# Kernel tuning notes

Measured on AMD Instinct MI355X. Metric: run time of the kernel, lower is better.

Reference implementation:

```python
import jax, jax.numpy as jnp
import numpy as np

DIM, C_HID, N_HEADS = 128, 32, 4
INF = 1.0e9
LN_EPS = 1e-5


def setup_inputs() -> dict:
    key = jax.random.key(0)
    ks = jax.random.split(key, 10)
    B, I, J, C, H, D = 1, 256, 256, DIM, N_HEADS, C_HID
    s = 0.02
    return {
        "x": jax.random.normal(ks[0], (B, I, J, C), jnp.float32),
        "mask": jnp.ones((B, I, J), jnp.float32),
        "ln_w": jnp.ones((C,), jnp.float32),
        "ln_b": jnp.zeros((C,), jnp.float32),
        "tri_w": jax.random.normal(ks[1], (C, H), jnp.float32) * s,  # bias=False
        "q_w": jax.random.normal(ks[2], (C, H * D), jnp.float32) * s,
        "k_w": jax.random.normal(ks[3], (C, H * D), jnp.float32) * s,
        "v_w": jax.random.normal(ks[4], (C, H * D), jnp.float32) * s,
        "g_w": jax.random.normal(ks[5], (C, H * D), jnp.float32) * s,
        "g_b": jnp.ones((H * D,), jnp.float32),  # gating init: bias=1
        "o_w": jax.random.normal(ks[6], (H * D, C), jnp.float32) * s,
        "o_b": jnp.zeros((C,), jnp.float32),
    }


def _layer_norm(x, w, b):
    mu = jnp.mean(x, axis=-1, keepdims=True)
    var = jnp.mean(jnp.square(x - mu), axis=-1, keepdims=True)
    return (x - mu) * jax.lax.rsqrt(var + LN_EPS) * w + b


def reference(x, mask, ln_w, ln_b, tri_w, q_w, k_w, v_w, g_w, g_b, o_w, o_b):
    # starting=True: no transpose. x: [B, I, J, C], mask: [B, I, J]
    B, I, J, C = x.shape
    H, D = N_HEADS, C_HID
    xn = _layer_norm(x, ln_w, ln_b)

    # mask bias: [B, I, 1, 1, J]; triangle bias: [B, 1, H, I(J), J]
    mask_bias = (INF * (mask - 1.0))[:, :, None, None, :]
    tri_bias = jnp.einsum("bijc,ch->bhij", xn, tri_w)[:, None]

    def proj(w):  # [B, I, H, J, D]
        return (xn @ w).reshape(B, I, J, H, D).transpose(0, 1, 3, 2, 4)

    q = proj(q_w) * (D ** -0.5)
    k = proj(k_w)
    v = proj(v_w)

    logits = jnp.einsum("bihqd,bihkd->bihqk", q, k) + mask_bias + tri_bias
    a = jax.nn.softmax(logits, axis=-1)
    o = jnp.einsum("bihqk,bihkd->bihqd", a, v).transpose(0, 1, 3, 2, 4)  # [B,I,J,H,D]

    g = jax.nn.sigmoid(xn @ g_w + g_b).reshape(B, I, J, H, D)
    o = (o * g).reshape(B, I, J, H * D)
    return o @ o_w + o_b
```

## Files before the change

### kernel.cpp

```cpp
#include <hip/hip_runtime.h>
#include <hip/hip_bf16.h>
#include <math.h>

#define LOG2E_ 1.4426950408889634f

typedef short short8 __attribute__((ext_vector_type(8)));
typedef float f32x4 __attribute__((ext_vector_type(4)));
typedef int int4v __attribute__((ext_vector_type(4)));

#if defined(__has_builtin)
#if __has_builtin(__builtin_amdgcn_exp2f)
#define EXP2F(x) __builtin_amdgcn_exp2f(x)
#else
#define EXP2F(x) exp2f(x)
#endif
#else
#define EXP2F(x) exp2f(x)
#endif

static __device__ __forceinline__ unsigned short f2bf(float f) {
    union { float f; unsigned int u; } c; c.f = f;
    c.u += 0x7fffu + ((c.u >> 16) & 1u);
    return (unsigned short)(c.u >> 16);
}
static __device__ __forceinline__ int pk2bf(float a, float b) {
    union { __hip_bfloat162 h; int i; } u;
    u.h = __float22bfloat162_rn(make_float2(a, b));
    return u.i;
}
static __device__ __forceinline__ void load_lds16(const void* g, void* l) {
    __builtin_amdgcn_global_load_lds(
        (const __attribute__((address_space(1))) void*)g,
        (__attribute__((address_space(3))) void*)l, 16, 0, 0);
}

__global__ __launch_bounds__(256) void ln_prep_kernel(
    const float* __restrict__ x, const float* __restrict__ ln_w,
    const float* __restrict__ ln_b, const float* __restrict__ tri_w,
    const float* __restrict__ qw, const float* __restrict__ kw,
    const float* __restrict__ vw, const float* __restrict__ gw,
    const float* __restrict__ ow,
    unsigned short* __restrict__ xn, float* __restrict__ triT,
    char* __restrict__ wimg)
{
    const int bid = blockIdx.x, tid = threadIdx.x;
    if (bid >= 8192) {
        int id = (bid - 8192) * 256 + tid;
        int h = id / 2688;
        int b = (id - h * 2688) * 16;
        unsigned short v[8];
        if (b < 32768) {
            int sl = b >> 13;
            int bi = b & 8191;
            int row = bi >> 8;
            int c8 = ((bi >> 4) & 15) ^ (row & 7);
            const float* src = (sl == 0) ? qw : (sl == 1) ? kw : (sl == 2) ? vw : gw;
            float scale = (sl == 0) ? (0.17677669529663687f * LOG2E_) : 1.0f;
            int R = h * 32 + row;
            #pragma unroll
            for (int e = 0; e < 8; ++e)
                v[e] = f2bf(src[(c8 * 8 + e) * 128 + R] * scale);
        } else {
            int o = b - 32768;
            int n = o / 80;
            int k8 = (o - n * 80) >> 4;
            if (k8 < 4) {
                #pragma unroll
                for (int e = 0; e < 8; ++e)
                    v[e] = f2bf(ow[(h * 32 + k8 * 8 + e) * 128 + n]);
            } else {
                #pragma unroll
                for (int e = 0; e < 8; ++e) v[e] = 0;
            }
        }
        *(short8*)(wimg + h * 43008 + b) = *(short8*)v;
        return;
    }

    const int row = bid * 8 + (tid >> 5);
    const int l = tid & 31;

    float4 xv = *(const float4*)(x + (size_t)row * 128 + l * 4);
    float s = (xv.x + xv.y) + (xv.z + xv.w);
    #pragma unroll
    for (int mk = 16; mk >= 1; mk >>= 1) s += __shfl_xor(s, mk, 64);
    float mu = s * (1.0f / 128.0f);

    float d0 = xv.x - mu, d1 = xv.y - mu, d2 = xv.z - mu, d3 = xv.w - mu;
    float sq = (d0 * d0 + d1 * d1) + (d2 * d2 + d3 * d3);
    #pragma unroll
    for (int mk = 16; mk >= 1; mk >>= 1) sq += __shfl_xor(sq, mk, 64);
    float rstd = rsqrtf(sq * (1.0f / 128.0f) + 1e-5f);

    float4 wv = *(const float4*)(ln_w + l * 4);
    float4 bv = *(const float4*)(ln_b + l * 4);
    float n0 = d0 * rstd * wv.x + bv.x;
    float n1 = d1 * rstd * wv.y + bv.y;
    float n2 = d2 * rstd * wv.z + bv.z;
    float n3 = d3 * rstd * wv.w + bv.w;

    ushort4 xo;
    xo.x = f2bf(n0); xo.y = f2bf(n1); xo.z = f2bf(n2); xo.w = f2bf(n3);
    *(ushort4*)(xn + (size_t)row * 128 + l * 4) = xo;

    float4 t0 = *(const float4*)(tri_w + (l * 4 + 0) * 4);
    float4 t1 = *(const float4*)(tri_w + (l * 4 + 1) * 4);
    float4 t2 = *(const float4*)(tri_w + (l * 4 + 2) * 4);
    float4 t3 = *(const float4*)(tri_w + (l * 4 + 3) * 4);
    float ax = (n0 * t0.x + n1 * t1.x) + (n2 * t2.x + n3 * t3.x);
    float ay = (n0 * t0.y + n1 * t1.y) + (n2 * t2.y + n3 * t3.y);
    float az = (n0 * t0.z + n1 * t1.z) + (n2 * t2.z + n3 * t3.z);
    float aw = (n0 * t0.w + n1 * t1.w) + (n2 * t2.w + n3 * t3.w);
    #pragma unroll
    for (int mk = 16; mk >= 1; mk >>= 1) {
        ax += __shfl_xor(ax, mk, 64);
        ay += __shfl_xor(ay, mk, 64);
        az += __shfl_xor(az, mk, 64);
        aw += __shfl_xor(aw, mk, 64);
    }
    if (l < 4) {
        float v = (l == 0) ? ax : (l == 1) ? ay : (l == 2) ? az : aw;
        int q = row >> 8, kc = row & 255;
        int off = l * 65536 + (q >> 4) * 4096 + (kc >> 4) * 256
                + (q & 15) * 16 + (kc & 15);
        triT[off] = v * LOG2E_;
    }
}

__global__ __launch_bounds__(1024, 4) void mega_kernel(
    const unsigned short* __restrict__ xn, const char* __restrict__ wimg,
    const float* __restrict__ g_b, const float* __restrict__ mask,
    const float* __restrict__ triT, const float* __restrict__ o_b,
    float* __restrict__ out)
{
    __shared__ __align__(16) char WBUF[2 * 43008];
    __shared__ __align__(16) unsigned short Qg[256 * 36];
    __shared__ __align__(16) unsigned short Kl[256 * 36];
    __shared__ __align__(16) unsigned short Vc[32 * 264];
    __shared__ float mb[256];

    const int i = blockIdx.x;
    const int tid = threadIdx.x;
    const int w = tid >> 6, lane = tid & 63, g = lane >> 4, m = lane & 15;
    const f32x4 zero = {0.f, 0.f, 0.f, 0.f};

    short8 xa[4];
    #pragma unroll
    for (int kc = 0; kc < 4; ++kc)
        xa[kc] = *(const short8*)(xn + (size_t)(i * 256 + w * 16 + m) * 128
                                  + kc * 32 + 8 * g);
    if (tid < 256) mb[tid] = (mask[i * 256 + tid] - 1.0f) * (1.0e9f * LOG2E_);

    {
        const char* src = wimg + w * 1024 + lane * 16;
        char* dst = WBUF + w * 1024;
        load_lds16(src, dst);
        load_lds16(src + 16384, dst + 16384);
        if (w < 10) load_lds16(src + 32768, dst + 32768);
    }
    __syncthreads();

    const int srcA = ((g & 1) << 1) | (g >> 1);
    const int idxA = (srcA * 16 + m) * 4;
    const int idxB = idxA ^ 64;
    const bool low = (lane < 32);
    const bool odd = (g & 1);
    const char* VcB0 = (const char*)Vc + m * 528;
    const char* VcB1 = (const char*)Vc + (16 + m) * 528;

    f32x4 oacc[8];
    #pragma unroll
    for (int nt = 0; nt < 8; ++nt) oacc[nt] = zero;

    const int qrow = w * 16 + m;

    #pragma unroll 1
    for (int h = 0; h < 4; ++h) {
        const char* wb = WBUF + (h & 1) * 43008;

        {
            f32x4 aq[2] = {zero, zero}, ak[2] = {zero, zero};
            #pragma unroll
            for (int kc = 0; kc < 4; ++kc) {
                short8 b0[2], b1[2];
                #pragma unroll
                for (int nt = 0; nt < 2; ++nt) {
                    int row = nt * 16 + m;
                    int off = (row * 256 + kc * 64 + 16 * g) ^ ((row & 7) << 4);
                    b0[nt] = *(const short8*)(wb + off);
                    b1[nt] = *(const short8*)(wb + 8192 + off);
                }
                __builtin_amdgcn_s_setprio(1);
                #pragma unroll
                for (int nt = 0; nt < 2; ++nt) {
                    aq[nt] = __builtin_amdgcn_mfma_f32_16x16x32_bf16(b0[nt], xa[kc], aq[nt], 0, 0, 0);
                    ak[nt] = __builtin_amdgcn_mfma_f32_16x16x32_bf16(b1[nt], xa[kc], ak[nt], 0, 0, 0);
                }
                __builtin_amdgcn_s_setprio(0);
            }
            #pragma unroll
            for (int nt = 0; nt < 2; ++nt) {
                int col = nt * 16 + 4 * g;
                ushort4 q4, k4;
                q4.x = f2bf(aq[nt][0]); q4.y = f2bf(aq[nt][1]);
                q4.z = f2bf(aq[nt][2]); q4.w = f2bf(aq[nt][3]);
                k4.x = f2bf(ak[nt][0]); k4.y = f2bf(ak[nt][1]);
                k4.z = f2bf(ak[nt][2]); k4.w = f2bf(ak[nt][3]);
                *(ushort4*)(Qg + qrow * 36 + col) = q4;
                *(ushort4*)(Kl + qrow * 36 + col) = k4;
            }
        }

        f32x4 gacc[2];
        {
            f32x4 av4[2] = {zero, zero}, ag[2] = {zero, zero};
            #pragma unroll
            for (int kc = 0; kc < 4; ++kc) {
                short8 b0[2], b1[2];
                #pragma unroll
                for (int nt = 0; nt < 2; ++nt) {
                    int row = nt * 16 + m;
                    int off = (row * 256 + kc * 64 + 16 * g) ^ ((row & 7) << 4);
                    b0[nt] = *(const short8*)(wb + 16384 + off);
                    b1[nt] = *(const short8*)(wb + 24576 + off);
                }
                __builtin_amdgcn_s_setprio(1);
                #pragma unroll
                for (int nt = 0; nt < 2; ++nt) {
                    av4[nt] = __builtin_amdgcn_mfma_f32_16x16x32_bf16(xa[kc], b0[nt], av4[nt], 0, 0, 0);
                    ag[nt]  = __builtin_amdgcn_mfma_f32_16x16x32_bf16(b1[nt], xa[kc], ag[nt], 0, 0, 0);
                }
                __builtin_amdgcn_s_setprio(0);
            }
            #pragma unroll
            for (int nt = 0; nt < 2; ++nt) {
                ushort4 v4;
                v4.x = f2bf(av4[nt][0]); v4.y = f2bf(av4[nt][1]);
                v4.z = f2bf(av4[nt][2]); v4.w = f2bf(av4[nt][3]);
                *(ushort4*)(Vc + (nt * 16 + m) * 264 + w * 16 + 4 * g) = v4;
                int col = nt * 16 + 4 * g;
                #pragma unroll
                for (int r = 0; r < 4; ++r)
                    gacc[nt][r] = 1.0f / (1.0f + __expf(-(ag[nt][r] + g_b[h * 32 + col + r])));
            }
        }
        __syncthreads();

        if (h < 3) {
            const char* src = wimg + (h + 1) * 43008 + w * 1024 + lane * 16;
            char* dst = WBUF + ((h + 1) & 1) * 43008 + w * 1024;
            load_lds16(src, dst);
            load_lds16(src + 16384, dst + 16384);
            if (w < 10) load_lds16(src + 32768, dst + 32768);
        }

        const short8 qf = *(const short8*)((const char*)Qg + qrow * 72 + 16 * g);
        const float* triQ = triT + h * 65536 + w * 4096 + m * 16 + 4 * g;

        float ls = 0.f;
        f32x4 o0 = zero, o1 = zero;

        #pragma unroll
        for (int c = 0; c < 8; ++c) {
            int d00, d01, d10, d11;
            {
                const int kt = 2 * c;
                short8 af = *(const short8*)((const char*)Kl + (kt * 16 + m) * 72 + 16 * g);
                f32x4 bias = *(const f32x4*)(mb + kt * 16 + 4 * g)
                           + *(const f32x4*)(triQ + kt * 256);
                __builtin_amdgcn_s_setprio(1);
                f32x4 acc = __builtin_amdgcn_mfma_f32_16x16x32_bf16(af, qf, bias, 0, 0, 0);
                __builtin_amdgcn_s_setprio(0);
                float p0 = EXP2F(acc[0]);
                float p1 = EXP2F(acc[1]);
                float p2 = EXP2F(acc[2]);
                float p3 = EXP2F(acc[3]);
                ls += (p0 + p1) + (p2 + p3);
                d00 = pk2bf(p0, p1); d01 = pk2bf(p2, p3);
            }
            {
                const int kt = 2 * c + 1;
                short8 af = *(const short8*)((const char*)Kl + (kt * 16 + m) * 72 + 16 * g);
                f32x4 bias = *(const f32x4*)(mb + kt * 16 + 4 * g)
                           + *(const f32x4*)(triQ + kt * 256);
                __builtin_amdgcn_s_setprio(1);
                f32x4 acc = __builtin_amdgcn_mfma_f32_16x16x32_bf16(af, qf, bias, 0, 0, 0);
                __builtin_amdgcn_s_setprio(0);
                float p0 = EXP2F(acc[0]);
                float p1 = EXP2F(acc[1]);
                float p2 = EXP2F(acc[2]);
                float p3 = EXP2F(acc[3]);
                ls += (p0 + p1) + (p2 + p3);
                d10 = pk2bf(p0, p1); d11 = pk2bf(p2, p3);
            }
            int pk0 = odd ? d10 : d00;
            int pk1 = odd ? d11 : d01;
            int pk2 = odd ? d00 : d10;
            int pk3 = odd ? d01 : d11;

            int dA0 = __builtin_amdgcn_ds_bpermute(idxA, pk0);
            int dA1 = __builtin_amdgcn_ds_bpermute(idxA, pk1);
            int dB0 = __builtin_amdgcn_ds_bpermute(idxB, pk2);
            int dB1 = __builtin_amdgcn_ds_bpermute(idxB, pk3);
            int4v bi;
            bi.x = low ? dA0 : dB0;
            bi.y = low ? dA1 : dB1;
            bi.z = low ? dB0 : dA0;
            bi.w = low ? dB1 : dA1;
            short8 bs = __builtin_bit_cast(short8, bi);

            short8 av0 = *(const short8*)(VcB0 + c * 64 + 16 * g);
            short8 av1 = *(const short8*)(VcB1 + c * 64 + 16 * g);
            __builtin_amdgcn_s_setprio(1);
            o0 = __builtin_amdgcn_mfma_f32_16x16x32_bf16(av0, bs, o0, 0, 0, 0);
            o1 = __builtin_amdgcn_mfma_f32_16x16x32_bf16(av1, bs, o1, 0, 0, 0);
            __builtin_amdgcn_s_setprio(0);
        }
        ls += __shfl_xor(ls, 16, 64);
        ls += __shfl_xor(ls, 32, 64);
        float inv = 1.0f / ls;

        ushort4 s0, s1;
        s0.x = f2bf(o0[0] * inv * gacc[0][0]);
        s0.y = f2bf(o0[1] * inv * gacc[0][1]);
        s0.z = f2bf(o0[2] * inv * gacc[0][2]);
        s0.w = f2bf(o0[3] * inv * gacc[0][3]);
        s1.x = f2bf(o1[0] * inv * gacc[1][0]);
        s1.y = f2bf(o1[1] * inv * gacc[1][1]);
        s1.z = f2bf(o1[2] * inv * gacc[1][2]);
        s1.w = f2bf(o1[3] * inv * gacc[1][3]);
        *(ushort4*)(Qg + qrow * 36 + 4 * g) = s0;
        *(ushort4*)(Qg + qrow * 36 + 16 + 4 * g) = s1;

        {
            short8 a = *(const short8*)((const char*)Qg + qrow * 72 + 16 * g);
            __builtin_amdgcn_s_setprio(1);
            #pragma unroll
            for (int nt = 0; nt < 8; ++nt) {
                short8 b = *(const short8*)(wb + 32768 + (nt * 16 + m) * 80 + 16 * g);
                oacc[nt] = __builtin_amdgcn_mfma_f32_16x16x32_bf16(b, a, oacc[nt], 0, 0, 0);
            }
            __builtin_amdgcn_s_setprio(0);
        }
        __syncthreads();
    }

    const int orow = i * 256 + qrow;
    #pragma unroll
    for (int nt = 0; nt < 8; ++nt) {
        int col = nt * 16 + 4 * g;
        float4 bv = *(const float4*)(o_b + col);
        float4 o;
        o.x = oacc[nt][0] + bv.x;
        o.y = oacc[nt][1] + bv.y;
        o.z = oacc[nt][2] + bv.z;
        o.w = oacc[nt][3] + bv.w;
        *(float4*)(out + (size_t)orow * 128 + col) = o;
    }
}

extern "C" void kernel_launch(void* const* d_in, const int* in_sizes, int n_in,
                              void* d_out, int out_size, void* d_ws, size_t ws_size,
                              hipStream_t stream) {
    (void)in_sizes; (void)n_in; (void)out_size; (void)ws_size;
    const float* x    = (const float*)d_in[0];
    const float* mask = (const float*)d_in[1];
    const float* ln_w = (const float*)d_in[2];
    const float* ln_b = (const float*)d_in[3];
    const float* tri_w= (const float*)d_in[4];
    const float* q_w  = (const float*)d_in[5];
    const float* k_w  = (const float*)d_in[6];
    const float* v_w  = (const float*)d_in[7];
    const float* g_w  = (const float*)d_in[8];
    const float* g_b  = (const float*)d_in[9];
    const float* o_w  = (const float*)d_in[10];
    const float* o_b  = (const float*)d_in[11];

    char* ws = (char*)d_ws;
    unsigned short* xn  = (unsigned short*)(ws);
    float*          tri = (float*)(ws + 16777216);
    char*           wimg= (char*)(ws + 17825792);

    ln_prep_kernel<<<8234, 256, 0, stream>>>(x, ln_w, ln_b, tri_w,
                                             q_w, k_w, v_w, g_w, o_w,
                                             xn, tri, wimg);
    mega_kernel<<<256, 1024, 0, stream>>>(xn, wimg, g_b, mask, tri, o_b,
                                          (float*)d_out);
}
```

Baseline: 69.74 us.

## Fuse layernorm and weight prep into mega kernel with cooperative grid sync

After: 111.4 us. +59.8%, slower.

```diff
diff --git a/kernel.cpp b/kernel.cpp
--- a/kernel.cpp
+++ b/kernel.cpp
@@ -1,6 +1,9 @@
 #include <hip/hip_runtime.h>
+#include <hip/hip_cooperative_groups.h>
 #include <hip/hip_bf16.h>
 #include <math.h>
+
+namespace cg = cooperative_groups;
 
 #define LOG2E_ 1.4426950408889634f
 
@@ -34,103 +37,15 @@
         (__attribute__((address_space(3))) void*)l, 16, 0, 0);
 }
 
-__global__ __launch_bounds__(256) void ln_prep_kernel(
-    const float* __restrict__ x, const float* __restrict__ ln_w,
-    const float* __restrict__ ln_b, const float* __restrict__ tri_w,
+__global__ __launch_bounds__(1024, 4) void mega_kernel(
+    const float* __restrict__ x, const float* __restrict__ mask,
+    const float* __restrict__ ln_w, const float* __restrict__ ln_b,
+    const float* __restrict__ tri_w,
     const float* __restrict__ qw, const float* __restrict__ kw,
     const float* __restrict__ vw, const float* __restrict__ gw,
     const float* __restrict__ ow,
-    unsigned short* __restrict__ xn, float* __restrict__ triT,
-    char* __restrict__ wimg)
-{
-    const int bid = blockIdx.x, tid = threadIdx.x;
-    if (bid >= 8192) {
-        int id = (bid - 8192) * 256 + tid;
-        int h = id / 2688;
-        int b = (id - h * 2688) * 16;
-        unsigned short v[8];
-        if (b < 32768) {
-            int sl = b >> 13;
-            int bi = b & 8191;
-            int row = bi >> 8;
-            int c8 = ((bi >> 4) & 15) ^ (row & 7);
-            const float* src = (sl == 0) ? qw : (sl == 1) ? kw : (sl == 2) ? vw : gw;
-            float scale = (sl == 0) ? (0.17677669529663687f * LOG2E_) : 1.0f;
-            int R = h * 32 + row;
-            #pragma unroll
-            for (int e = 0; e < 8; ++e)
-                v[e] = f2bf(src[(c8 * 8 + e) * 128 + R] * scale);
-        } else {
-            int o = b - 32768;
-            int n = o / 80;
-            int k8 = (o - n * 80) >> 4;
-            if (k8 < 4) {
-                #pragma unroll
-                for (int e = 0; e < 8; ++e)
-                    v[e] = f2bf(ow[(h * 32 + k8 * 8 + e) * 128 + n]);
-            } else {
-                #pragma unroll
-                for (int e = 0; e < 8; ++e) v[e] = 0;
-            }
-        }
-        *(short8*)(wimg + h * 43008 + b) = *(short8*)v;
-        return;
-    }
-
-    const int row = bid * 8 + (tid >> 5);
-    const int l = tid & 31;
-
-    float4 xv = *(const float4*)(x + (size_t)row * 128 + l * 4);
-    float s = (xv.x + xv.y) + (xv.z + xv.w);
-    #pragma unroll
-    for (int mk = 16; mk >= 1; mk >>= 1) s += __shfl_xor(s, mk, 64);
-    float mu = s * (1.0f / 128.0f);
-
-    float d0 = xv.x - mu, d1 = xv.y - mu, d2 = xv.z - mu, d3 = xv.w - mu;
-    float sq = (d0 * d0 + d1 * d1) + (d2 * d2 + d3 * d3);
-    #pragma unroll
-    for (int mk = 16; mk >= 1; mk >>= 1) sq += __shfl_xor(sq, mk, 64);
-    float rstd = rsqrtf(sq * (1.0f / 128.0f) + 1e-5f);
-
-    float4 wv = *(const float4*)(ln_w + l * 4);
-    float4 bv = *(const float4*)(ln_b + l * 4);
-    float n0 = d0 * rstd * wv.x + bv.x;
-    float n1 = d1 * rstd * wv.y + bv.y;
-    float n2 = d2 * rstd * wv.z + bv.z;
-    float n3 = d3 * rstd * wv.w + bv.w;
-
-    ushort4 xo;
-    xo.x = f2bf(n0); xo.y = f2bf(n1); xo.z = f2bf(n2); xo.w = f2bf(n3);
-    *(ushort4*)(xn + (size_t)row * 128 + l * 4) = xo;
-
-    float4 t0 = *(const float4*)(tri_w + (l * 4 + 0) * 4);
-    float4 t1 = *(const float4*)(tri_w + (l * 4 + 1) * 4);
-    float4 t2 = *(const float4*)(tri_w + (l * 4 + 2) * 4);
-    float4 t3 = *(const float4*)(tri_w + (l * 4 + 3) * 4);
-    float ax = (n0 * t0.x + n1 * t1.x) + (n2 * t2.x + n3 * t3.x);
-    float ay = (n0 * t0.y + n1 * t1.y) + (n2 * t2.y + n3 * t3.y);
-    float az = (n0 * t0.z + n1 * t1.z) + (n2 * t2.z + n3 * t3.z);
-    float aw = (n0 * t0.w + n1 * t1.w) + (n2 * t2.w + n3 * t3.w);
-    #pragma unroll
-    for (int mk = 16; mk >= 1; mk >>= 1) {
-        ax += __shfl_xor(ax, mk, 64);
-        ay += __shfl_xor(ay, mk, 64);
-        az += __shfl_xor(az, mk, 64);
-        aw += __shfl_xor(aw, mk, 64);
-    }
-    if (l < 4) {
-        float v = (l == 0) ? ax : (l == 1) ? ay : (l == 2) ? az : aw;
-        int q = row >> 8, kc = row & 255;
-        int off = l * 65536 + (q >> 4) * 4096 + (kc >> 4) * 256
-                + (q & 15) * 16 + (kc & 15);
-        triT[off] = v * LOG2E_;
-    }
-}
-
-__global__ __launch_bounds__(1024, 4) void mega_kernel(
-    const unsigned short* __restrict__ xn, const char* __restrict__ wimg,
-    const float* __restrict__ g_b, const float* __restrict__ mask,
-    const float* __restrict__ triT, const float* __restrict__ o_b,
+    const float* __restrict__ g_b, const float* __restrict__ o_b,
+    float* __restrict__ triT, char* __restrict__ wimg,
     float* __restrict__ out)
 {
     __shared__ __align__(16) char WBUF[2 * 43008];
@@ -138,18 +53,105 @@
     __shared__ __align__(16) unsigned short Kl[256 * 36];
     __shared__ __align__(16) unsigned short Vc[32 * 264];
     __shared__ float mb[256];
+    unsigned short* Xs = (unsigned short*)WBUF;
 
     const int i = blockIdx.x;
     const int tid = threadIdx.x;
     const int w = tid >> 6, lane = tid & 63, g = lane >> 4, m = lane & 15;
     const f32x4 zero = {0.f, 0.f, 0.f, 0.f};
 
+    {
+        int id = i * 1024 + tid;
+        if (id < 10752) {
+            int h = id / 2688;
+            int b = (id - h * 2688) * 16;
+            unsigned short v[8];
+            if (b < 32768) {
+                int sl = b >> 13;
+                int bi = b & 8191;
+                int row = bi >> 8;
+                int c8 = ((bi >> 4) & 15) ^ (row & 7);
+                const float* src = (sl == 0) ? qw : (sl == 1) ? kw
+                                 : (sl == 2) ? vw : gw;
+                float scale = (sl == 0) ? (0.17677669529663687f * LOG2E_) : 1.0f;
+                int R = h * 32 + row;
+                #pragma unroll
+                for (int e = 0; e < 8; ++e)
+                    v[e] = f2bf(src[(c8 * 8 + e) * 128 + R] * scale);
+            } else {
+                int o = b - 32768;
+                int n = o / 80;
+                int k8 = (o - n * 80) >> 4;
+                if (k8 < 4) {
+                    #pragma unroll
+                    for (int e = 0; e < 8; ++e)
+                        v[e] = f2bf(ow[(h * 32 + k8 * 8 + e) * 128 + n]);
+                } else {
+                    #pragma unroll
+                    for (int e = 0; e < 8; ++e) v[e] = 0;
+                }
+            }
+            *(short8*)(wimg + h * 43008 + b) = *(short8*)v;
+        }
+    }
+    if (tid < 256) mb[tid] = (mask[i * 256 + tid] - 1.0f) * (1.0e9f * LOG2E_);
+
+    {
+        const int j = tid >> 2, ql = tid & 3;
+        const float* xr = x + ((size_t)i * 256 + j) * 128 + ql * 32;
+
+        float s = 0.f, s2 = 0.f;
+        #pragma unroll
+        for (int c8 = 0; c8 < 8; ++c8) {
+            float4 v = *(const float4*)(xr + c8 * 4);
+            s  += (v.x + v.y) + (v.z + v.w);
+            s2 += (v.x * v.x + v.y * v.y) + (v.z * v.z + v.w * v.w);
+        }
+        s  += __shfl_xor(s, 1, 64);  s  += __shfl_xor(s, 2, 64);
+        s2 += __shfl_xor(s2, 1, 64); s2 += __shfl_xor(s2, 2, 64);
+        float mu = s * (1.0f / 128.0f);
+        float rstd = rsqrtf(fmaxf(s2 * (1.0f / 128.0f) - mu * mu, 0.f) + 1e-5f);
+
+        float th0 = 0.f, th1 = 0.f, th2 = 0.f, th3 = 0.f;
+        #pragma unroll
+        for (int c8 = 0; c8 < 8; ++c8) {
+            float4 v  = *(const float4*)(xr + c8 * 4);
+            float4 wv = *(const float4*)(ln_w + ql * 32 + c8 * 4);
+            float4 bv = *(const float4*)(ln_b + ql * 32 + c8 * 4);
+            float n0 = (v.x - mu) * rstd * wv.x + bv.x;
+            float n1 = (v.y - mu) * rstd * wv.y + bv.y;
+            float n2 = (v.z - mu) * rstd * wv.z + bv.z;
+            float n3 = (v.w - mu) * rstd * wv.w + bv.w;
+            ushort4 o;
+            o.x = f2bf(n0); o.y = f2bf(n1); o.z = f2bf(n2); o.w = f2bf(n3);
+            *(ushort4*)(Xs + j * 128 + ql * 32 + c8 * 4) = o;
+            const float* tw = tri_w + (ql * 32 + c8 * 4) * 4;
+            float4 t0 = *(const float4*)(tw);
+            float4 t1 = *(const float4*)(tw + 4);
+            float4 t2 = *(const float4*)(tw + 8);
+            float4 t3 = *(const float4*)(tw + 12);
+            th0 += n0 * t0.x + n1 * t1.x + n2 * t2.x + n3 * t3.x;
+            th1 += n0 * t0.y + n1 * t1.y + n2 * t2.y + n3 * t3.y;
+            th2 += n0 * t0.z + n1 * t1.z + n2 * t2.z + n3 * t3.z;
+            th3 += n0 * t0.w + n1 * t1.w + n2 * t2.w + n3 * t3.w;
+        }
+        th0 += __shfl_xor(th0, 1, 64); th0 += __shfl_xor(th0, 2, 64);
+        th1 += __shfl_xor(th1, 1, 64); th1 += __shfl_xor(th1, 2, 64);
+        th2 += __shfl_xor(th2, 1, 64); th2 += __shfl_xor(th2, 2, 64);
+        th3 += __shfl_xor(th3, 1, 64); th3 += __shfl_xor(th3, 2, 64);
+        float tv = (ql == 0) ? th0 : (ql == 1) ? th1 : (ql == 2) ? th2 : th3;
+        int off = ql * 65536 + (i >> 4) * 4096 + (j >> 4) * 256
+                + (i & 15) * 16 + (j & 15);
+        triT[off] = tv * LOG2E_;
+    }
+    __syncthreads();
+
     short8 xa[4];
     #pragma unroll
     for (int kc = 0; kc < 4; ++kc)
-        xa[kc] = *(const short8*)(xn + (size_t)(i * 256 + w * 16 + m) * 128
-                                  + kc * 32 + 8 * g);
-    if (tid < 256) mb[tid] = (mask[i * 256 + tid] - 1.0f) * (1.0e9f * LOG2E_);
+        xa[kc] = *(const short8*)(Xs + (w * 16 + m) * 128 + kc * 32 + 8 * g);
+
+    cg::this_grid().sync();
 
     {
         const char* src = wimg + w * 1024 + lane * 16;
@@ -377,13 +379,15 @@
     const float* o_b  = (const float*)d_in[11];
 
     char* ws = (char*)d_ws;
-    unsigned short* xn  = (unsigned short*)(ws);
-    float*          tri = (float*)(ws + 16777216);
-    char*           wimg= (char*)(ws + 17825792);
-
-    ln_prep_kernel<<<8234, 256, 0, stream>>>(x, ln_w, ln_b, tri_w,
-                                             q_w, k_w, v_w, g_w, o_w,
-                                             xn, tri, wimg);
-    mega_kernel<<<256, 1024, 0, stream>>>(xn, wimg, g_b, mask, tri, o_b,
-                                          (float*)d_out);
-}
+    float* tri  = (float*)ws;
+    char*  wimg = ws + 1048576;
+    float* outp = (float*)d_out;
+
+    void* args[] = {
+        (void*)&x, (void*)&mask, (void*)&ln_w, (void*)&ln_b, (void*)&tri_w,
+        (void*)&q_w, (void*)&k_w, (void*)&v_w, (void*)&g_w, (void*)&o_w,
+        (void*)&g_b, (void*)&o_b, (void*)&tri, (void*)&wimg, (void*)&outp
+    };
+    hipLaunchCooperativeKernel((const void*)mega_kernel, dim3(256), dim3(1024),
+                               args, 0, stream);
+}
```
